# Optimization experiments

Hardware: AMD Instinct MI355X
Metric: run time of the kernel (lower is better)

The kernel has to match this reference:

```python
import jax, jax.numpy as jnp
import numpy as np
import math

B, T, C, H = 2, 2048, 1024, 16
HD = C // H  # head dim = 64

def setup_inputs() -> dict:
    key = jax.random.key(0)
    ks = jax.random.split(key, 5)
    s = 1.0 / math.sqrt(C)
    return {
        "x": jax.random.normal(ks[0], (B, T, C), jnp.float32),
        "Wq": jax.random.normal(ks[1], (C, C), jnp.float32) * s,
        "bq": jnp.zeros((C,), jnp.float32),
        "Wk": jax.random.normal(ks[2], (C, C), jnp.float32) * s,
        "bk": jnp.zeros((C,), jnp.float32),
        "Wv": jax.random.normal(ks[3], (C, C), jnp.float32) * s,
        "bv": jnp.zeros((C,), jnp.float32),
        "Wp": jax.random.normal(ks[4], (C, C), jnp.float32) * s,
        "bp": jnp.zeros((C,), jnp.float32),
    }

def reference(x, Wq, bq, Wk, bk, Wv, bv, Wp, bp):
    # project and split heads: [B,T,C] -> [B,H,T,HD]
    def heads(y):
        return y.reshape(B, T, H, HD).transpose(0, 2, 1, 3)
    q = heads(x @ Wq + bq)
    k = heads(x @ Wk + bk)
    v = heads(x @ Wv + bv)
    scale = 1.0 / math.sqrt(HD)
    att = jnp.einsum('bhqd,bhkd->bhqk', q, k) * scale  # [B,H,T,T]
    causal = jnp.tril(jnp.ones((T, T), bool))
    att = jnp.where(causal, att, -jnp.inf)
    att = jax.nn.softmax(att, axis=-1)  # attention_dropout p=0 -> identity
    y = jnp.einsum('bhqk,bhkd->bhqd', att, v)  # [B,H,T,HD]
    y = y.transpose(0, 2, 1, 3).reshape(B, T, C)
    return y @ Wp + bp  # residual_dropout p=0 -> identity
```

## Files before the change

kernel.cpp:

```cpp
#include <hip/hip_runtime.h>
#include <hip/hip_bf16.h>
#include <stdint.h>

typedef __bf16 bf16x8 __attribute__((ext_vector_type(8)));
typedef __bf16 bf16x4 __attribute__((ext_vector_type(4)));
typedef float  f32x4  __attribute__((ext_vector_type(4)));

#define MFMA16(a, b, c) __builtin_amdgcn_mfma_f32_16x16x32_bf16(a, b, c, 0, 0, 0)

#if __has_builtin(__builtin_amdgcn_exp2f)
#define EXP2(x) __builtin_amdgcn_exp2f(x)
#else
#define EXP2(x) exp2f(x)
#endif

__device__ __forceinline__ void ld16(void* lds, const void* g) {
    __builtin_amdgcn_global_load_lds(
        (const __attribute__((address_space(1))) void*)(uintptr_t)g,
        (__attribute__((address_space(3))) void*)(uint32_t)(uintptr_t)lds,
        16, 0, 0);
}

__global__ __launch_bounds__(256) void convert_bf16(const float* __restrict__ src,
                                                    __bf16* __restrict__ dst) {
    int i = (blockIdx.x * 256 + threadIdx.x) * 4;
    float4 v = *(const float4*)(src + i);
    dst[i]     = (__bf16)v.x;
    dst[i + 1] = (__bf16)v.y;
    dst[i + 2] = (__bf16)v.z;
    dst[i + 3] = (__bf16)v.w;
}

__global__ __launch_bounds__(1024) void transpose_w(const float* __restrict__ W0,
                                                    const float* __restrict__ W1,
                                                    const float* __restrict__ W2,
                                                    const float* __restrict__ W3,
                                                    __bf16* __restrict__ dst) {
    __shared__ __bf16 t[32][33];
    const int z = blockIdx.z;
    const float* W = (z == 0) ? W0 : (z == 1) ? W1 : (z == 2) ? W2 : W3;
    __bf16* D = dst + (size_t)z * 1048576;
    const int tx = threadIdx.x, ty = threadIdx.y;
    t[ty][tx] = (__bf16)W[(size_t)(blockIdx.y * 32 + ty) * 1024 + blockIdx.x * 32 + tx];
    __syncthreads();
    D[(size_t)(blockIdx.x * 32 + ty) * 1024 + blockIdx.y * 32 + tx] = t[tx][ty];
}

__device__ __forceinline__ void gemm_mainloop(const __bf16* __restrict__ A,
                                              const __bf16* __restrict__ BT,
                                              int K, __bf16* As, __bf16* Bs,
                                              f32x4 acc[4][4]) {
    const int tid  = threadIdx.x;
    const int lane = tid & 63;
    const int wid  = tid >> 6;
    const int quad = lane >> 4;
    const int l16  = lane & 15;
    const int wm   = wid >> 1;
    const int wn   = wid & 1;

    const int srow = wid * 16 + (lane >> 2);
    const int scol = (lane & 3) * 8;
    const int sdst = wid * 512 + lane * 8;

    for (int k0 = 0; k0 < K; k0 += 32) {
        ld16(As + sdst,        A  + (size_t)srow        * K + k0 + scol);
        ld16(As + 2048 + sdst, A  + (size_t)(srow + 64) * K + k0 + scol);
        ld16(Bs + sdst,        BT + (size_t)srow        * K + k0 + scol);
        ld16(Bs + 2048 + sdst, BT + (size_t)(srow + 64) * K + k0 + scol);
        __syncthreads();
        bf16x8 af[4], bf[4];
#pragma unroll
        for (int mt = 0; mt < 4; mt++)
            af[mt] = *(const bf16x8*)(As + (wm * 64 + mt * 16 + l16) * 32 + quad * 8);
#pragma unroll
        for (int nt = 0; nt < 4; nt++)
            bf[nt] = *(const bf16x8*)(Bs + (wn * 64 + nt * 16 + l16) * 32 + quad * 8);
#pragma unroll
        for (int mt = 0; mt < 4; mt++)
#pragma unroll
            for (int nt = 0; nt < 4; nt++)
                acc[mt][nt] = MFMA16(af[mt], bf[nt], acc[mt][nt]);
        __syncthreads();
    }
}

__global__ __launch_bounds__(256) void qkv_gemm(const __bf16* __restrict__ X,
                                                const __bf16* __restrict__ WTb,
                                                const float* __restrict__ b0,
                                                const float* __restrict__ b1,
                                                const float* __restrict__ b2,
                                                __bf16* __restrict__ qk,
                                                __bf16* __restrict__ vt) {
    __shared__ __attribute__((aligned(16))) __bf16 As[4096];
    __shared__ __attribute__((aligned(16))) __bf16 Bs[4096];
    const int z = blockIdx.z;
    const __bf16* BT   = WTb + (size_t)z * 1048576;
    const float* bias  = (z == 0) ? b0 : (z == 1) ? b1 : b2;
    const int m0 = blockIdx.y * 128, n0 = blockIdx.x * 128;
    f32x4 acc[4][4];
    const f32x4 zz = {0.f, 0.f, 0.f, 0.f};
#pragma unroll
    for (int i = 0; i < 4; i++)
#pragma unroll
        for (int j = 0; j < 4; j++) acc[i][j] = zz;
    gemm_mainloop(X + (size_t)m0 * 1024, BT + (size_t)n0 * 1024, 1024, As, Bs, acc);

    const int lane = threadIdx.x & 63, wid = threadIdx.x >> 6;
    const int quad = lane >> 4, l16 = lane & 15, wm = wid >> 1, wn = wid & 1;
    if (z == 2) {
#pragma unroll
        for (int nt = 0; nt < 4; nt++) {
            int col = n0 + wn * 64 + nt * 16 + l16;
            float bv = bias[col];
            int h = col >> 6, hd = col & 63;
#pragma unroll
            for (int mt = 0; mt < 4; mt++) {
                int m = m0 + wm * 64 + mt * 16 + quad * 4;
                int b = m >> 11, tt = m & 2047;
                bf16x4 pk;
                pk.x = (__bf16)(acc[mt][nt].x + bv);
                pk.y = (__bf16)(acc[mt][nt].y + bv);
                pk.z = (__bf16)(acc[mt][nt].z + bv);
                pk.w = (__bf16)(acc[mt][nt].w + bv);
                *(bf16x4*)(vt + ((size_t)((b * 16 + h) * 64 + hd)) * 2048 + tt) = pk;
            }
        }
    } else {
        const float sq = (z == 0) ? 0.18033688011112042f : 1.0f;
        __bf16* dst = qk + (size_t)z * 4194304;
#pragma unroll
        for (int nt = 0; nt < 4; nt++) {
            int col = n0 + wn * 64 + nt * 16 + l16;
            float bv = bias[col];
            int h = col >> 6, hd = col & 63;
#pragma unroll
            for (int mt = 0; mt < 4; mt++) {
#pragma unroll
                for (int r4 = 0; r4 < 4; r4++) {
                    int m = m0 + wm * 64 + mt * 16 + quad * 4 + r4;
                    int b = m >> 11, tt = m & 2047;
                    float v = (acc[mt][nt][r4] + bv) * sq;
                    dst[((size_t)((b * 16 + h) * 2048 + tt)) * 64 + hd] = (__bf16)v;
                }
            }
        }
    }
}

__global__ __launch_bounds__(256) void proj_gemm(const __bf16* __restrict__ Yw,
                                                 const __bf16* __restrict__ WT,
                                                 const float* __restrict__ bias,
                                                 float* __restrict__ out) {
    __shared__ __attribute__((aligned(16))) __bf16 As[4096];
    __shared__ __attribute__((aligned(16))) __bf16 Bs[4096];
    const int m0 = blockIdx.y * 128, n0 = blockIdx.x * 128;
    f32x4 acc[4][4];
    const f32x4 zz = {0.f, 0.f, 0.f, 0.f};
#pragma unroll
    for (int i = 0; i < 4; i++)
#pragma unroll
        for (int j = 0; j < 4; j++) acc[i][j] = zz;
    gemm_mainloop(Yw + (size_t)m0 * 1024, WT + (size_t)n0 * 1024, 1024, As, Bs, acc);

    const int lane = threadIdx.x & 63, wid = threadIdx.x >> 6;
    const int quad = lane >> 4, l16 = lane & 15, wm = wid >> 1, wn = wid & 1;
#pragma unroll
    for (int nt = 0; nt < 4; nt++) {
        int col = n0 + wn * 64 + nt * 16 + l16;
        float bv = bias[col];
#pragma unroll
        for (int mt = 0; mt < 4; mt++) {
#pragma unroll
            for (int r4 = 0; r4 < 4; r4++) {
                int m = m0 + wm * 64 + mt * 16 + quad * 4 + r4;
                out[(size_t)m * 1024 + col] = acc[mt][nt][r4] + bv;
            }
        }
    }
}

__global__ __launch_bounds__(256, 1) void attn_kernel(const __bf16* __restrict__ Qg,
                                                      const __bf16* __restrict__ Kg,
                                                      const __bf16* __restrict__ Vtg,
                                                      __bf16* __restrict__ Y) {
    __shared__ __attribute__((aligned(16))) __bf16 Kb[2][128 * 64];
    __shared__ __attribute__((aligned(16))) __bf16 Vb[2][64 * 128];
    __shared__ __attribute__((aligned(16))) __bf16 Ps[4][32 * 136];
    __shared__ __attribute__((aligned(16))) float  Lw[4][32];

    const int tid  = threadIdx.x;
    const int lane = tid & 63;
    const int wid  = tid >> 6;
    const int quad = lane >> 4;
    const int l16  = lane & 15;
    const int bkid = blockIdx.x;
    const int head  = ((bkid & 7) << 2) + ((bkid >> 3) & 3);
    const int ipair = bkid >> 5;
    const size_t hbase = (size_t)head * (2048 * 64);
    const f32x4 zz = {0.f, 0.f, 0.f, 0.f};

    const int kr  = lane >> 3;
    const int kc8 = (lane & 7) ^ kr;
    const int vr  = lane >> 4;
    const int vl  = lane & 15;

#pragma unroll 1
    for (int itm = 0; itm < 2; itm++) {
        const int qi  = itm ? (15 - ipair) : ipair;
        const int ktl = qi;
        const int q0  = qi << 7;
        const int q0w = q0 + wid * 32;

        bf16x8 qf[2][2];
#pragma unroll
        for (int nt = 0; nt < 2; nt++)
#pragma unroll
            for (int kk = 0; kk < 2; kk++)
                qf[nt][kk] = *(const bf16x8*)(Qg + hbase +
                                              (size_t)(q0w + nt * 16 + l16) * 64 +
                                              kk * 32 + quad * 8);

        f32x4 acc_o[2][4];
#pragma unroll
        for (int i = 0; i < 2; i++)
#pragma unroll
            for (int jj = 0; jj < 4; jj++) acc_o[i][jj] = zz;
        float l_s[2] = {0.f, 0.f};

        auto stage = [&](int bf, int key0) {
#pragma unroll
            for (int i = 0; i < 4; i++) {
                const int c = wid * 4 + i;
                ld16((char*)&Kb[bf][0] + c * 1024 + lane * 16,
                     Kg + hbase + (size_t)(key0 + c * 8 + kr) * 64 + kc8 * 8);
            }
#pragma unroll
            for (int i = 0; i < 4; i++) {
                const int c = wid * 4 + i;
                const int row = c * 4 + vr;
                const int vc  = vl ^ (row & 7);
                ld16((char*)&Vb[bf][0] + c * 1024 + lane * 16,
                     Vtg + hbase + (size_t)row * 2048 + key0 + vc * 8);
            }
        };

        stage(0, 0);
        __syncthreads();
        int buf = 0;

#pragma unroll 1
        for (int kt = 0; kt <= ktl; kt++) {
            if (kt < ktl) stage(buf ^ 1, (kt + 1) << 7);

            f32x4 accs[8][2];
#pragma unroll
            for (int mt = 0; mt < 8; mt++) { accs[mt][0] = zz; accs[mt][1] = zz; }
#pragma unroll
            for (int kk = 0; kk < 2; kk++) {
#pragma unroll
                for (int mt = 0; mt < 8; mt++) {
                    bf16x8 kf = *(const bf16x8*)(&Kb[buf][(mt * 16 + l16) * 64 +
                                                 (((kk * 4 + quad) ^ (l16 & 7)) << 3)]);
                    accs[mt][0] = MFMA16(kf, qf[0][kk], accs[mt][0]);
                    accs[mt][1] = MFMA16(kf, qf[1][kk], accs[mt][1]);
                }
            }

            if (kt == ktl) {
#pragma unroll
                for (int mt = 0; mt < 8; mt++)
#pragma unroll
                    for (int nt = 0; nt < 2; nt++) {
                        int q_g = wid * 32 + nt * 16 + l16;
#pragma unroll
                        for (int r4 = 0; r4 < 4; r4++) {
                            int key_g = mt * 16 + quad * 4 + r4;
                            if (key_g > q_g) accs[mt][nt][r4] = -1e30f;
                        }
                    }
            }

            float s_s[2] = {0.f, 0.f};
#pragma unroll
            for (int mt = 0; mt < 8; mt++)
#pragma unroll
                for (int nt = 0; nt < 2; nt++) {
                    f32x4 pv;
                    pv.x = EXP2(accs[mt][nt].x);
                    pv.y = EXP2(accs[mt][nt].y);
                    pv.z = EXP2(accs[mt][nt].z);
                    pv.w = EXP2(accs[mt][nt].w);
                    s_s[nt] += (pv.x + pv.y) + (pv.z + pv.w);
                    bf16x4 pk;
                    pk.x = (__bf16)pv.x; pk.y = (__bf16)pv.y;
                    pk.z = (__bf16)pv.z; pk.w = (__bf16)pv.w;
                    *(bf16x4*)(&Ps[wid][(nt * 16 + l16) * 136 + mt * 16 + quad * 4]) = pk;
                }
#pragma unroll
            for (int nt = 0; nt < 2; nt++) {
                float t = s_s[nt];
                t += __shfl_xor(t, 16);
                t += __shfl_xor(t, 32);
                l_s[nt] += t;
            }

#pragma unroll
            for (int kk = 0; kk < 4; kk++) {
                bf16x8 pf[2], vf[4];
#pragma unroll
                for (int mtP = 0; mtP < 2; mtP++)
                    pf[mtP] = *(const bf16x8*)(&Ps[wid][(mtP * 16 + l16) * 136 +
                                                        kk * 32 + quad * 8]);
#pragma unroll
                for (int nv = 0; nv < 4; nv++)
                    vf[nv] = *(const bf16x8*)(&Vb[buf][(nv * 16 + l16) * 128 +
                                              (((kk * 4 + quad) ^ (l16 & 7)) << 3)]);
#pragma unroll
                for (int mtP = 0; mtP < 2; mtP++)
#pragma unroll
                    for (int nv = 0; nv < 4; nv++)
                        acc_o[mtP][nv] = MFMA16(pf[mtP], vf[nv], acc_o[mtP][nv]);
            }

            __syncthreads();
            buf ^= 1;
        }

        if (quad == 0) { Lw[wid][l16] = l_s[0]; Lw[wid][16 + l16] = l_s[1]; }
        float* Om = (float*)&Ps[wid][0];
#pragma unroll
        for (int mtP = 0; mtP < 2; mtP++)
#pragma unroll
            for (int nv = 0; nv < 4; nv++)
#pragma unroll
                for (int r4 = 0; r4 < 4; r4++)
                    Om[(mtP * 16 + quad * 4 + r4) * 68 + nv * 16 + l16] =
                        acc_o[mtP][nv][r4];
        __syncthreads();

        {
            const int q  = lane >> 1;
            const int d0 = (lane & 1) * 32;
            float li = 1.0f / Lw[wid][q];
            f32x4 s[8];
#pragma unroll
            for (int jj = 0; jj < 8; jj++)
                s[jj] = *(const f32x4*)(&Om[q * 68 + d0 + jj * 4]);
            bf16x8 o0, o1;
#pragma unroll
            for (int e = 0; e < 4; e++) {
                o0[e]     = (__bf16)(s[0][e] * li); o0[e + 4] = (__bf16)(s[1][e] * li);
                o1[e]     = (__bf16)(s[4][e] * li); o1[e + 4] = (__bf16)(s[5][e] * li);
            }
#pragma unroll
            for (int e = 0; e < 4; e++) {
            }
            o0[0] = (__bf16)(s[0][0] * li); o0[1] = (__bf16)(s[0][1] * li);
            o0[2] = (__bf16)(s[0][2] * li); o0[3] = (__bf16)(s[0][3] * li);
            o0[4] = (__bf16)(s[1][0] * li); o0[5] = (__bf16)(s[1][1] * li);
            o0[6] = (__bf16)(s[1][2] * li); o0[7] = (__bf16)(s[1][3] * li);
            o1[0] = (__bf16)(s[2][0] * li); o1[1] = (__bf16)(s[2][1] * li);
            o1[2] = (__bf16)(s[2][2] * li); o1[3] = (__bf16)(s[2][3] * li);
            o1[4] = (__bf16)(s[3][0] * li); o1[5] = (__bf16)(s[3][1] * li);
            o1[6] = (__bf16)(s[3][2] * li); o1[7] = (__bf16)(s[3][3] * li);
            bf16x8 o2, o3;
            o2[0] = (__bf16)(s[4][0] * li); o2[1] = (__bf16)(s[4][1] * li);
            o2[2] = (__bf16)(s[4][2] * li); o2[3] = (__bf16)(s[4][3] * li);
            o2[4] = (__bf16)(s[5][0] * li); o2[5] = (__bf16)(s[5][1] * li);
            o2[6] = (__bf16)(s[5][2] * li); o2[7] = (__bf16)(s[5][3] * li);
            o3[0] = (__bf16)(s[6][0] * li); o3[1] = (__bf16)(s[6][1] * li);
            o3[2] = (__bf16)(s[6][2] * li); o3[3] = (__bf16)(s[6][3] * li);
            o3[4] = (__bf16)(s[7][0] * li); o3[5] = (__bf16)(s[7][1] * li);
            o3[6] = (__bf16)(s[7][2] * li); o3[7] = (__bf16)(s[7][3] * li);
            const int bb = head >> 4, hh = head & 15;
            __bf16* yp = Y + ((size_t)(bb * 2048 + q0w + q)) * 1024 + hh * 64 + d0;
            *(bf16x8*)(yp)      = o0;
            *(bf16x8*)(yp + 8)  = o1;
            *(bf16x8*)(yp + 16) = o2;
            *(bf16x8*)(yp + 24) = o3;
        }
        __syncthreads();
    }
}

#define XB_OFF  0
#define WT_OFF  4194304
#define Q_OFF   8388608
#define K_OFF   12582912
#define VT_OFF  16777216
#define Y_OFF   0

extern "C" void kernel_launch(void* const* d_in, const int* in_sizes, int n_in,
                              void* d_out, int out_size, void* d_ws, size_t ws_size,
                              hipStream_t stream) {
    const float* x  = (const float*)d_in[0];
    const float* Wq = (const float*)d_in[1];
    const float* bq = (const float*)d_in[2];
    const float* Wk = (const float*)d_in[3];
    const float* bk = (const float*)d_in[4];
    const float* Wv = (const float*)d_in[5];
    const float* bv = (const float*)d_in[6];
    const float* Wp = (const float*)d_in[7];
    const float* bp = (const float*)d_in[8];
    __bf16* ws  = (__bf16*)d_ws;
    float*  out = (float*)d_out;
    if (ws_size < (size_t)41943040) return;

    convert_bf16<<<4096, 256, 0, stream>>>(x, ws + XB_OFF);
    transpose_w<<<dim3(32, 32, 4), dim3(32, 32), 0, stream>>>(Wq, Wk, Wv, Wp, ws + WT_OFF);
    qkv_gemm<<<dim3(8, 32, 3), 256, 0, stream>>>(ws + XB_OFF, ws + WT_OFF, bq, bk, bv,
                                                 ws + Q_OFF, ws + VT_OFF);
    attn_kernel<<<dim3(256), 256, 0, stream>>>(ws + Q_OFF, ws + K_OFF, ws + VT_OFF,
                                               ws + Y_OFF);
    proj_gemm<<<dim3(8, 32), 256, 0, stream>>>(ws + Y_OFF, ws + WT_OFF + 3 * 1048576, bp, out);
}
```

Measured before the change: 209.1 us.

## Fuse input conversion into weight transpose and remap GEMM block order

Folds the x float-to-bf16 conversion into the weight-transpose kernel as an extra grid slice, removing one kernel launch. Both GEMMs now use a flat 1D grid with a remapped block-to-tile order. The order groups blocks by XCD (o&7) so tiles that share A rows and B columns run on the same chiplet, aiming at better L2 reuse. Also drops dead duplicate bf16 packing code in the attention epilogue. The remapping depends on the assumed round-robin dispatch of blocks across XCDs.

After: 188.3 us. -10.0%, faster.

```diff
diff --git a/kernel.cpp b/kernel.cpp
--- a/kernel.cpp
+++ b/kernel.cpp
@@ -21,26 +21,28 @@
         16, 0, 0);
 }
 
-__global__ __launch_bounds__(256) void convert_bf16(const float* __restrict__ src,
-                                                    __bf16* __restrict__ dst) {
-    int i = (blockIdx.x * 256 + threadIdx.x) * 4;
-    float4 v = *(const float4*)(src + i);
-    dst[i]     = (__bf16)v.x;
-    dst[i + 1] = (__bf16)v.y;
-    dst[i + 2] = (__bf16)v.z;
-    dst[i + 3] = (__bf16)v.w;
-}
-
-__global__ __launch_bounds__(1024) void transpose_w(const float* __restrict__ W0,
+__global__ __launch_bounds__(1024) void prep_kernel(const float* __restrict__ x,
+                                                    const float* __restrict__ W0,
                                                     const float* __restrict__ W1,
                                                     const float* __restrict__ W2,
                                                     const float* __restrict__ W3,
-                                                    __bf16* __restrict__ dst) {
+                                                    __bf16* __restrict__ wdst,
+                                                    __bf16* __restrict__ xdst) {
     __shared__ __bf16 t[32][33];
     const int z = blockIdx.z;
+    const int tx = threadIdx.x, ty = threadIdx.y;
+    if (z == 4) {
+        int blin = blockIdx.y * 32 + blockIdx.x;
+        int i = (blin * 1024 + ty * 32 + tx) * 4;
+        float4 v = *(const float4*)(x + i);
+        xdst[i]     = (__bf16)v.x;
+        xdst[i + 1] = (__bf16)v.y;
+        xdst[i + 2] = (__bf16)v.z;
+        xdst[i + 3] = (__bf16)v.w;
+        return;
+    }
     const float* W = (z == 0) ? W0 : (z == 1) ? W1 : (z == 2) ? W2 : W3;
-    __bf16* D = dst + (size_t)z * 1048576;
-    const int tx = threadIdx.x, ty = threadIdx.y;
+    __bf16* D = wdst + (size_t)z * 1048576;
     t[ty][tx] = (__bf16)W[(size_t)(blockIdx.y * 32 + ty) * 1024 + blockIdx.x * 32 + tx];
     __syncthreads();
     D[(size_t)(blockIdx.x * 32 + ty) * 1024 + blockIdx.y * 32 + tx] = t[tx][ty];
@@ -93,10 +95,15 @@
                                                 __bf16* __restrict__ vt) {
     __shared__ __attribute__((aligned(16))) __bf16 As[4096];
     __shared__ __attribute__((aligned(16))) __bf16 Bs[4096];
-    const int z = blockIdx.z;
+    const int o  = blockIdx.x;
+    const int g  = o & 7, r = o >> 3;
+    const int mB = ((g >> 1) << 3) + (r & 7);
+    const int nz = (g & 1) * 12 + (r >> 3);
+    const int z  = nz >> 3;
+    const int n  = nz & 7;
     const __bf16* BT   = WTb + (size_t)z * 1048576;
     const float* bias  = (z == 0) ? b0 : (z == 1) ? b1 : b2;
-    const int m0 = blockIdx.y * 128, n0 = blockIdx.x * 128;
+    const int m0 = mB * 128, n0 = n * 128;
     f32x4 acc[4][4];
     const f32x4 zz = {0.f, 0.f, 0.f, 0.f};
 #pragma unroll
@@ -153,7 +160,10 @@
                                                  float* __restrict__ out) {
     __shared__ __attribute__((aligned(16))) __bf16 As[4096];
     __shared__ __attribute__((aligned(16))) __bf16 Bs[4096];
-    const int m0 = blockIdx.y * 128, n0 = blockIdx.x * 128;
+    const int o = blockIdx.x;
+    const int g = o & 7, r = o >> 3;
+    const int m0 = (g * 4 + (r & 3)) * 128;
+    const int n0 = (r >> 2) * 128;
     f32x4 acc[4][4];
     const f32x4 zz = {0.f, 0.f, 0.f, 0.f};
 #pragma unroll
@@ -346,15 +356,7 @@
 #pragma unroll
             for (int jj = 0; jj < 8; jj++)
                 s[jj] = *(const f32x4*)(&Om[q * 68 + d0 + jj * 4]);
-            bf16x8 o0, o1;
-#pragma unroll
-            for (int e = 0; e < 4; e++) {
-                o0[e]     = (__bf16)(s[0][e] * li); o0[e + 4] = (__bf16)(s[1][e] * li);
-                o1[e]     = (__bf16)(s[4][e] * li); o1[e + 4] = (__bf16)(s[5][e] * li);
-            }
-#pragma unroll
-            for (int e = 0; e < 4; e++) {
-            }
+            bf16x8 o0, o1, o2, o3;
             o0[0] = (__bf16)(s[0][0] * li); o0[1] = (__bf16)(s[0][1] * li);
             o0[2] = (__bf16)(s[0][2] * li); o0[3] = (__bf16)(s[0][3] * li);
             o0[4] = (__bf16)(s[1][0] * li); o0[5] = (__bf16)(s[1][1] * li);
@@ -363,7 +365,6 @@
             o1[2] = (__bf16)(s[2][2] * li); o1[3] = (__bf16)(s[2][3] * li);
             o1[4] = (__bf16)(s[3][0] * li); o1[5] = (__bf16)(s[3][1] * li);
             o1[6] = (__bf16)(s[3][2] * li); o1[7] = (__bf16)(s[3][3] * li);
-            bf16x8 o2, o3;
             o2[0] = (__bf16)(s[4][0] * li); o2[1] = (__bf16)(s[4][1] * li);
             o2[2] = (__bf16)(s[4][2] * li); o2[3] = (__bf16)(s[4][3] * li);
             o2[4] = (__bf16)(s[5][0] * li); o2[5] = (__bf16)(s[5][1] * li);
@@ -406,11 +407,11 @@
     float*  out = (float*)d_out;
     if (ws_size < (size_t)41943040) return;
 
-    convert_bf16<<<4096, 256, 0, stream>>>(x, ws + XB_OFF);
-    transpose_w<<<dim3(32, 32, 4), dim3(32, 32), 0, stream>>>(Wq, Wk, Wv, Wp, ws + WT_OFF);
-    qkv_gemm<<<dim3(8, 32, 3), 256, 0, stream>>>(ws + XB_OFF, ws + WT_OFF, bq, bk, bv,
-                                                 ws + Q_OFF, ws + VT_OFF);
+    prep_kernel<<<dim3(32, 32, 5), dim3(32, 32), 0, stream>>>(x, Wq, Wk, Wv, Wp,
+                                                              ws + WT_OFF, ws + XB_OFF);
+    qkv_gemm<<<dim3(768), 256, 0, stream>>>(ws + XB_OFF, ws + WT_OFF, bq, bk, bv,
+                                            ws + Q_OFF, ws + VT_OFF);
     attn_kernel<<<dim3(256), 256, 0, stream>>>(ws + Q_OFF, ws + K_OFF, ws + VT_OFF,
                                                ws + Y_OFF);
-    proj_gemm<<<dim3(8, 32), 256, 0, stream>>>(ws + Y_OFF, ws + WT_OFF + 3 * 1048576, bp, out);
-}
+    proj_gemm<<<dim3(256), 256, 0, stream>>>(ws + Y_OFF, ws + WT_OFF + 3 * 1048576, bp, out);
+}
```
